# Performance work log

Measured on AMD Instinct MI355X. Metric: run time of the kernel, lower is better.

Reference implementation:

```python
import jax, jax.numpy as jnp
import numpy as np

N_EMBD = 1024
N_HEAD = 16
HEAD_DIM = N_EMBD // N_HEAD
BLOCK_SIZE = 2048
ROPE_BASE = 10000.0


def _rope_tables(dim, max_len, base=ROPE_BASE):
    half = dim // 2
    freqs = 1.0 / base ** (jnp.arange(half, dtype=jnp.float32) / half)
    angles = jnp.arange(max_len, dtype=jnp.float32)[:, None] * freqs[None, :]  # (T, half)
    return jnp.cos(angles), jnp.sin(angles)


def _apply_rope(x, cos, sin):
    # x: (B, H, T, D); cos/sin: (T, D//2)
    T = x.shape[2]
    c = cos[:T][None, None]
    s = sin[:T][None, None]
    x1 = x[..., ::2]
    x2 = x[..., 1::2]
    out = jnp.stack([x1 * c - x2 * s, x1 * s + x2 * c], axis=-1)  # (B,H,T,D//2,2)
    return out.reshape(x.shape)


def setup_inputs() -> dict:
    key = jax.random.key(0)
    k1, k2, k3, k4, k5 = jax.random.split(key, 5)
    B, T, C = 2, 2048, N_EMBD
    x = jax.random.normal(k1, (B, T, C), dtype=jnp.float32)
    scale = 1.0 / np.sqrt(C)
    Wqkv = jax.random.normal(k2, (C, 3 * C), dtype=jnp.float32) * scale
    bqkv = jax.random.normal(k3, (3 * C,), dtype=jnp.float32) * 0.01
    Wproj = jax.random.normal(k4, (C, C), dtype=jnp.float32) * scale
    bproj = jax.random.normal(k5, (C,), dtype=jnp.float32) * 0.01
    cos, sin = _rope_tables(HEAD_DIM, BLOCK_SIZE)
    return {"x": x, "Wqkv": Wqkv, "bqkv": bqkv, "Wproj": Wproj, "bproj": bproj,
            "cos": cos, "sin": sin}


def reference(x, Wqkv, bqkv, Wproj, bproj, cos, sin):
    B, T, C = x.shape
    H, D = N_HEAD, HEAD_DIM
    qkv = x @ Wqkv + bqkv  # (B,T,3C)
    q, k, v = jnp.split(qkv, 3, axis=-1)
    # (B,T,C) -> (B,H,T,D)
    q = q.reshape(B, T, H, D).transpose(0, 2, 1, 3)
    k = k.reshape(B, T, H, D).transpose(0, 2, 1, 3)
    v = v.reshape(B, T, H, D).transpose(0, 2, 1, 3)
    q = _apply_rope(q, cos, sin)
    k = _apply_rope(k, cos, sin)
    att = jnp.einsum('bhtd,bhsd->bhts', q, k) * (D ** -0.5)
    causal = jnp.tril(jnp.ones((T, T), dtype=bool))
    att = jnp.where(causal[None, None], att, -jnp.inf)
    att = jax.nn.softmax(att, axis=-1)
    y = jnp.einsum('bhts,bhsd->bhtd', att, v)  # (B,H,T,D)
    y = y.transpose(0, 2, 1, 3).reshape(B, T, C)
    return y @ Wproj + bproj
```

## Files before the change

### kernel.cpp

```cpp
#include <hip/hip_runtime.h>
#include <stdint.h>

typedef short s16x8 __attribute__((ext_vector_type(8)));
typedef float f32x4 __attribute__((ext_vector_type(4)));
typedef unsigned short u16;
typedef unsigned int u32;

__device__ __forceinline__ float bf2f(u16 u) {
  union { u32 i; float f; } v; v.i = ((u32)u) << 16; return v.f;
}
__device__ __forceinline__ u16 f2bf(float f) {
  union { float f; u32 i; } v; v.f = f;
  u32 i = v.i;
  return (u16)((i + 0x7fffu + ((i >> 16) & 1u)) >> 16);
}
__device__ __forceinline__ u16 f2bf_fast(float f) {
  union { float f; u32 i; } v; v.f = f;
  return (u16)((v.i + 0x8000u) >> 16);
}

__device__ __forceinline__ s16x8 load8(const void* p, size_t idx, int isf32) {
  s16x8 r;
  if (isf32) {
    const float* f = (const float*)p + idx;
    f32x4 a = *(const f32x4*)f;
    f32x4 b = *(const f32x4*)(f + 4);
#pragma unroll
    for (int j = 0; j < 4; j++) {
      r[j] = (short)f2bf(a[j]);
      r[4 + j] = (short)f2bf(b[j]);
    }
  } else {
    r = *(const s16x8*)((const u16*)p + idx);
  }
  return r;
}
__device__ __forceinline__ float loadf(const void* p, size_t idx, int isf32) {
  return isf32 ? ((const float*)p)[idx] : bf2f(((const u16*)p)[idx]);
}

__device__ __forceinline__ void cp16(const u16* g, u16* l) {
  __builtin_amdgcn_global_load_lds(
      (const __attribute__((address_space(1))) u32*)g,
      (__attribute__((address_space(3))) u32*)l, 16, 0, 0);
}

__global__ void detect_dtype(const u16* __restrict__ x, int* __restrict__ flags) {
  int cnt = 0;
  for (int i = threadIdx.x; i < 4096; i += 64) {
    int e = (x[i] >> 7) & 0xFF;
    if (e >= 0xF0) cnt++;
  }
  unsigned long long any = __ballot(cnt > 0);
  if (threadIdx.x == 0) {
    flags[0] = (any != 0ull) ? 1 : 0;
    flags[1] = 0;
  }
}

__global__ __launch_bounds__(256) void convert_x(const void* __restrict__ x,
                                                 const int* __restrict__ fp,
                                                 u16* __restrict__ xb) {
  int tid = blockIdx.x * 256 + threadIdx.x;
  int r = tid & 127, kq = (tid >> 7) & 3, kB = (tid >> 9) & 31, mB = tid >> 14;
  size_t src = (size_t)(mB * 128 + r) * 1024 + kB * 32 + kq * 8;
  *(s16x8*)(xb + (size_t)tid * 8) = load8(x, src, *fp);
}

__global__ __launch_bounds__(256) void transposeW2(
    const void* __restrict__ Wqkv, const void* __restrict__ Wproj,
    const int* __restrict__ fp, u16* __restrict__ WqkvT,
    u16* __restrict__ WprojT) {
  __shared__ u32 tile32[32 * 66];
  const int f = *fp;
  const int tid = threadIdx.x;
  const int bx = blockIdx.x;
  const void* W;
  u16* WT;
  int N, nb, qkvSide;
  if (bx < 48) { W = Wqkv; WT = WqkvT; N = 3072; nb = bx * 64; qkvSide = 1; }
  else         { W = Wproj; WT = WprojT; N = 1024; nb = (bx - 48) * 64; qkvSide = 0; }
  const int kb = blockIdx.y * 64;
  {
    int a = tid >> 3, c8 = tid & 7;
    s16x8 r0 = load8(W, (size_t)(kb + 2 * a) * N + nb + c8 * 8, f);
    s16x8 r1 = load8(W, (size_t)(kb + 2 * a + 1) * N + nb + c8 * 8, f);
#pragma unroll
    for (int j = 0; j < 8; j++)
      tile32[a * 66 + c8 * 8 + j] = (u32)(u16)r0[j] | ((u32)(u16)r1[j] << 16);
  }
  __syncthreads();
#pragma unroll
  for (int i = 0; i < 2; i++) {
    int idx = tid + i * 256;
    int n = idx & 63, c8 = idx >> 6;
    s16x8 v;
#pragma unroll
    for (int w = 0; w < 4; w++) {
      u32 pk = tile32[(c8 * 4 + w) * 66 + n];
      v[2 * w] = (short)(u16)(pk & 0xFFFF);
      v[2 * w + 1] = (short)(u16)(pk >> 16);
    }
    int R = nb + n, k = kb + c8 * 8;
    int kB = k >> 5, kq = (k >> 3) & 3;
    size_t off;
    if (qkvSide) {
      int nB = R >> 7, r = R & 127;
      off = ((size_t)(nB * 32 + kB) * 4 + kq) * 1024 + r * 8;
    } else {
      int nB = R >> 6, r = R & 63;
      off = (size_t)(nB * 32 + kB) * 2048 + kq * 512 + r * 8;
    }
    *(s16x8*)(WT + off) = v;
  }
}

__global__ __launch_bounds__(256) void transposeV(const u16* __restrict__ qkv,
                                                  u16* __restrict__ vT) {
  __shared__ u32 tile32[64 * 33];
  const int tid = threadIdx.x;
  const int tb = blockIdx.x * 64, bh = blockIdx.y;
  const int b = bh >> 4, h = bh & 15;
  {
    int a = tid >> 3, c8 = tid & 7;
    const u16* base = qkv + (size_t)(b * 2048 + tb + 2 * a) * 3072 + 2048 + h * 64;
    s16x8 r0 = *(const s16x8*)(base + c8 * 8);
    s16x8 r1 = *(const s16x8*)(base + 3072 + c8 * 8);
#pragma unroll
    for (int j = 0; j < 8; j++)
      tile32[(c8 * 8 + j) * 33 + a] = (u32)(u16)r0[j] | ((u32)(u16)r1[j] << 16);
  }
  __syncthreads();
#pragma unroll
  for (int i = 0; i < 2; i++) {
    int idx = tid + i * 256;
    int d = idx >> 3, c8 = idx & 7;
    s16x8 v;
#pragma unroll
    for (int w = 0; w < 4; w++) {
      u32 pk = tile32[d * 33 + c8 * 4 + w];
      v[2 * w] = (short)(u16)(pk & 0xFFFF);
      v[2 * w + 1] = (short)(u16)(pk >> 16);
    }
    *(s16x8*)(vT + ((size_t)bh * 64 + d) * 2048 + tb + c8 * 8) = v;
  }
}

template <int NT, int KK, int ATILED>
__global__ __launch_bounds__(256) void gemm_bt(
    const u16* __restrict__ A, int lda, const u16* __restrict__ Bt,
    const void* __restrict__ bias, const int* __restrict__ fI32,
    void* __restrict__ C, int ropeMode, int outF,
    const void* __restrict__ cost, const void* __restrict__ sint, int N) {
  constexpr int NTW = NT / 32;
  constexpr int KT = KK / 32;
  constexpr int TB = NT * 32;
  __shared__ __attribute__((aligned(16))) u16 As[128 * 32];
  __shared__ __attribute__((aligned(16))) u16 Bs[NT * 32];
  const int inf32 = *fI32;
  const int tid = threadIdx.x;
  const int wave = tid >> 6, lane = tid & 63, quad = lane >> 4, l16 = lane & 15;
  const int m0 = blockIdx.y * 128, n0 = blockIdx.x * NT;
  const int wm = (wave & 1) * 64, wn = (wave >> 1) * (NT / 2);
  f32x4 acc[4][NTW];
#pragma unroll
  for (int i = 0; i < 4; i++)
#pragma unroll
    for (int j = 0; j < NTW; j++) acc[i][j] = (f32x4){0.f, 0.f, 0.f, 0.f};

  const u16* aT = nullptr;
  const u16* aP = nullptr;
  if constexpr (ATILED) {
    aT = A + (size_t)blockIdx.y * KT * 4096 + wave * 1024 + lane * 8;
  } else {
    const int lr = lane >> 2, lk = (lane & 3) * 8;
    aP = A + (size_t)(m0 + wave * 32 + lr) * lda + lk;
  }
  const u16* bT = Bt + (size_t)blockIdx.x * KT * TB + wave * (NT / 64) * 512 +
                  lane * 8;

  for (int kB = 0; kB < KT; ++kB) {
    __syncthreads();
    if constexpr (ATILED) {
      cp16(aT + (size_t)kB * 4096, As + wave * 1024);
      cp16(aT + (size_t)kB * 4096 + 512, As + wave * 1024 + 512);
    } else {
      const int kb = kB * 32;
      cp16(aP + kb, As + wave * 32 * 32);
      cp16(aP + kb + (size_t)16 * lda, As + wave * 32 * 32 + 16 * 32);
    }
#pragma unroll
    for (int i = 0; i < NT / 64; i++)
      cp16(bT + (size_t)kB * TB + i * 512,
           Bs + (wave * (NT / 64) + i) * 512);
    __syncthreads();
    s16x8 af[4], bfr[NTW];
#pragma unroll
    for (int tt = 0; tt < 4; tt++) {
      if constexpr (ATILED)
        af[tt] = *(const s16x8*)(As + quad * 1024 + (wm + tt * 16 + l16) * 8);
      else
        af[tt] = *(const s16x8*)(As + (wm + tt * 16 + l16) * 32 + quad * 8);
    }
#pragma unroll
    for (int tt = 0; tt < NTW; tt++)
      bfr[tt] = *(const s16x8*)(Bs + quad * (NT * 8) + (wn + tt * 16 + l16) * 8);
#pragma unroll
    for (int mt = 0; mt < 4; mt++)
#pragma unroll
      for (int nt = 0; nt < NTW; nt++)
        acc[mt][nt] = __builtin_amdgcn_mfma_f32_16x16x32_bf16(
            af[mt], bfr[nt], acc[mt][nt], 0, 0, 0);
  }

#pragma unroll
  for (int nt = 0; nt < NTW; nt++) {
    int col = n0 + wn + nt * 16 + l16;
    float bv = loadf(bias, col, inf32);
    if (ropeMode && col < 2048) {
      int j = (col & 63) >> 1, odd = col & 1;
#pragma unroll
      for (int mt = 0; mt < 4; mt++)
#pragma unroll
        for (int r = 0; r < 4; r++) {
          int row = m0 + wm + mt * 16 + quad * 4 + r, t = row & 2047;
          float cv = loadf(cost, (size_t)t * 32 + j, inf32);
          float sv = loadf(sint, (size_t)t * 32 + j, inf32);
          float val = acc[mt][nt][r] + bv;
          float pr = __shfl_xor(val, 1);
          float res = odd ? (pr * sv + val * cv) : (val * cv - pr * sv);
          ((u16*)C)[(size_t)row * N + col] = f2bf(res);
        }
    } else if (outF && inf32) {
#pragma unroll
      for (int mt = 0; mt < 4; mt++)
#pragma unroll
        for (int r = 0; r < 4; r++) {
          int row = m0 + wm + mt * 16 + quad * 4 + r;
          ((float*)C)[(size_t)row * N + col] = acc[mt][nt][r] + bv;
        }
    } else {
#pragma unroll
      for (int mt = 0; mt < 4; mt++)
#pragma unroll
        for (int r = 0; r < 4; r++) {
          int row = m0 + wm + mt * 16 + quad * 4 + r;
          ((u16*)C)[(size_t)row * N + col] = f2bf(acc[mt][nt][r] + bv);
        }
    }
  }
}

__global__ __launch_bounds__(512) void attn_kernel(u16* qkv,
                                                   const u16* __restrict__ vT) {
  __shared__ __attribute__((aligned(16))) u16 Ks[64 * 72];
  __shared__ __attribute__((aligned(16))) u16 Vt[64 * 72];
  __shared__ __attribute__((aligned(16))) u16 Pl[8][16 * 72];
  const int tid = threadIdx.x;
  const int wave = tid >> 6, lane = tid & 63, quad = lane >> 4, l16 = lane & 15;
  const int cu = blockIdx.x & 255, round = blockIdx.x >> 8;
  const int p = cu >> 5, bh = cu & 31;
  const int qt = round ? p : 15 - p;
  const int h = bh & 15;
  const size_t rb = (size_t)(bh >> 4) * 2048;
  const int qb = qt * 128;
  const float SCALE = 0.18033688011112042f;

  s16x8 qa0, qa1;
  {
    const u16* qp = qkv + (rb + qb + wave * 16 + l16) * 3072 + h * 64;
    qa0 = *(const s16x8*)(qp + quad * 8);
    qa1 = *(const s16x8*)(qp + 32 + quad * 8);
  }

  f32x4 o[4];
  float l_r[4] = {0.f, 0.f, 0.f, 0.f};
#pragma unroll
  for (int i = 0; i < 4; i++) o[i] = (f32x4){0.f, 0.f, 0.f, 0.f};

  const int nchunks = 2 * qt + 2;
  const int srow = tid >> 3, sc8 = tid & 7;
  s16x8 kr, vr;
  {
    kr = *(const s16x8*)(qkv + (rb + srow) * 3072 + 1024 + h * 64 + sc8 * 8);
    vr = *(const s16x8*)(vT + ((size_t)bh * 64 + srow) * 2048 + sc8 * 8);
  }

  for (int c = 0; c < nchunks; c++) {
    const int sb = c * 64;
    __syncthreads();
    *(s16x8*)(Ks + srow * 72 + sc8 * 8) = kr;
    *(s16x8*)(Vt + srow * 72 + sc8 * 8) = vr;
    __syncthreads();
    if (c + 1 < nchunks) {
      const int nb = sb + 64;
      kr = *(const s16x8*)(qkv + (rb + nb + srow) * 3072 + 1024 + h * 64 +
                           sc8 * 8);
      vr = *(const s16x8*)(vT + ((size_t)bh * 64 + srow) * 2048 + nb + sc8 * 8);
    }

    if (sb > qb + wave * 16 + 15) continue;

    f32x4 S[4];
#pragma unroll
    for (int kf = 0; kf < 4; kf++) {
      s16x8 k0 = *(const s16x8*)(Ks + (kf * 16 + l16) * 72 + quad * 8);
      s16x8 k1 = *(const s16x8*)(Ks + (kf * 16 + l16) * 72 + 32 + quad * 8);
      f32x4 a = (f32x4){0.f, 0.f, 0.f, 0.f};
      a = __builtin_amdgcn_mfma_f32_16x16x32_bf16(qa0, k0, a, 0, 0, 0);
      a = __builtin_amdgcn_mfma_f32_16x16x32_bf16(qa1, k1, a, 0, 0, 0);
      S[kf] = a;
    }

    u16* P = Pl[wave];
    const int mq = qb + wave * 16;
    const bool needMask = (sb + 63) > mq;
#pragma unroll
    for (int r = 0; r < 4; r++) {
      const int qi = mq + quad * 4 + r;
#pragma unroll
      for (int kf = 0; kf < 4; kf++) {
        float pv = __builtin_amdgcn_exp2f(S[kf][r] * SCALE);
        if (needMask) pv = ((sb + kf * 16 + l16) <= qi) ? pv : 0.f;
        l_r[r] += pv;
        P[(quad * 4 + r) * 72 + kf * 16 + l16] = f2bf_fast(pv);
      }
    }
    asm volatile("s_waitcnt lgkmcnt(0)" ::: "memory");
    s16x8 pa0 = *(const s16x8*)(P + l16 * 72 + quad * 8);
    s16x8 pa1 = *(const s16x8*)(P + l16 * 72 + 32 + quad * 8);

#pragma unroll
    for (int dt = 0; dt < 4; dt++) {
      s16x8 vb0 = *(const s16x8*)(Vt + (dt * 16 + l16) * 72 + quad * 8);
      s16x8 vb1 = *(const s16x8*)(Vt + (dt * 16 + l16) * 72 + 32 + quad * 8);
      o[dt] = __builtin_amdgcn_mfma_f32_16x16x32_bf16(pa0, vb0, o[dt], 0, 0, 0);
      o[dt] = __builtin_amdgcn_mfma_f32_16x16x32_bf16(pa1, vb1, o[dt], 0, 0, 0);
    }
  }

  float inv[4];
#pragma unroll
  for (int r = 0; r < 4; r++) {
    float rs = l_r[r];
#pragma unroll
    for (int off = 8; off; off >>= 1) rs += __shfl_xor(rs, off);
    inv[r] = 1.0f / fmaxf(rs, 1e-30f);
  }
#pragma unroll
  for (int dt = 0; dt < 4; dt++)
#pragma unroll
    for (int r = 0; r < 4; r++)
      qkv[(rb + qb + wave * 16 + quad * 4 + r) * 3072 + 2048 + h * 64 +
          dt * 16 + l16] = f2bf(o[dt][r] * inv[r]);
}

extern "C" void kernel_launch(void* const* d_in, const int* in_sizes, int n_in,
                              void* d_out, int out_size, void* d_ws,
                              size_t ws_size, hipStream_t stream) {
  const void* x = d_in[0];
  const void* Wqkv = d_in[1];
  const void* bqkv = d_in[2];
  const void* Wproj = d_in[3];
  const void* bproj = d_in[4];
  const void* cost = d_in[5];
  const void* sint = d_in[6];

  int* flags = (int*)d_ws;
  u16* WqkvT = (u16*)d_ws + 128;
  u16* WprojT = WqkvT + (size_t)3072 * 1024;
  u16* qkv = WprojT + (size_t)1024 * 1024;
  u16* yb = qkv + 2048;
  u16* xb = (u16*)d_out;
  u16* vT = (u16*)d_out + (size_t)4096 * 1024;

  detect_dtype<<<1, 64, 0, stream>>>((const u16*)x, flags);
  convert_x<<<2048, 256, 0, stream>>>(x, flags, xb);
  transposeW2<<<dim3(64, 16), 256, 0, stream>>>(Wqkv, Wproj, flags, WqkvT,
                                                WprojT);
  gemm_bt<128, 1024, 1><<<dim3(24, 32), 256, 0, stream>>>(
      xb, 1024, WqkvT, bqkv, flags, qkv, 1, 0, cost, sint, 3072);
  transposeV<<<dim3(32, 32), 256, 0, stream>>>(qkv, vT);
  attn_kernel<<<512, 512, 0, stream>>>(qkv, vT);
  gemm_bt<64, 1024, 0><<<dim3(16, 32), 256, 0, stream>>>(
      yb, 3072, WprojT, bproj, flags, d_out, 0, 1, nullptr, nullptr, 1024);
}
```

Measured before the change: 218.3 us.

## Double-buffer GEMM LDS tiles and remap blocks per XCD for locality

Converts the GEMM K-loop to a double-buffered LDS pipeline: the async copy for the next K-slice is issued before computing the current one, with explicit vmcnt waits and barriers in place of two __syncthreads per iteration. It also remaps the linear block ID so that blocks assigned round-robin to each of the 8 XCDs cover a contiguous region of the output grid, aiming for better L2 reuse of A and B tiles. LDS use doubles, which may reduce occupancy. The hand-written vmcnt counts and the grid remap both assume particular shapes: the grid must divide into 2x4 regions, and the counts must match the number of cp16 instructions issued per stage.

```diff
diff --git a/kernel.cpp b/kernel.cpp
--- a/kernel.cpp
+++ b/kernel.cpp
@@ -155,12 +155,21 @@
   constexpr int NTW = NT / 32;
   constexpr int KT = KK / 32;
   constexpr int TB = NT * 32;
-  __shared__ __attribute__((aligned(16))) u16 As[128 * 32];
-  __shared__ __attribute__((aligned(16))) u16 Bs[NT * 32];
+  __shared__ __attribute__((aligned(16))) u16 As[2][128 * 32];
+  __shared__ __attribute__((aligned(16))) u16 Bs[2][NT * 32];
   const int inf32 = *fI32;
   const int tid = threadIdx.x;
   const int wave = tid >> 6, lane = tid & 63, quad = lane >> 4, l16 = lane & 15;
-  const int m0 = blockIdx.y * 128, n0 = blockIdx.x * NT;
+
+  const int GX = gridDim.x;
+  const int lin = blockIdx.y * GX + blockIdx.x;
+  const int xcd = lin & 7, idx = lin >> 3;
+  const int RX = GX >> 1, RY = gridDim.y >> 2;
+  const int sx = idx % RX, sy = idx / RX;
+  const int bx = (xcd & 1) * RX + sx;
+  const int by = (xcd >> 1) * RY + sy;
+
+  const int m0 = by * 128, n0 = bx * NT;
   const int wm = (wave & 1) * 64, wn = (wave >> 1) * (NT / 2);
   f32x4 acc[4][NTW];
 #pragma unroll
@@ -171,46 +180,67 @@
   const u16* aT = nullptr;
   const u16* aP = nullptr;
   if constexpr (ATILED) {
-    aT = A + (size_t)blockIdx.y * KT * 4096 + wave * 1024 + lane * 8;
+    aT = A + (size_t)by * KT * 4096 + wave * 1024 + lane * 8;
   } else {
     const int lr = lane >> 2, lk = (lane & 3) * 8;
     aP = A + (size_t)(m0 + wave * 32 + lr) * lda + lk;
   }
-  const u16* bT = Bt + (size_t)blockIdx.x * KT * TB + wave * (NT / 64) * 512 +
+  const u16* bT = Bt + (size_t)bx * KT * TB + wave * (NT / 64) * 512 +
                   lane * 8;
 
-  for (int kB = 0; kB < KT; ++kB) {
-    __syncthreads();
+  auto STAGE = [&](int kB, u16* ad, u16* bd) {
     if constexpr (ATILED) {
-      cp16(aT + (size_t)kB * 4096, As + wave * 1024);
-      cp16(aT + (size_t)kB * 4096 + 512, As + wave * 1024 + 512);
+      cp16(aT + (size_t)kB * 4096, ad + wave * 1024);
+      cp16(aT + (size_t)kB * 4096 + 512, ad + wave * 1024 + 512);
     } else {
       const int kb = kB * 32;
-      cp16(aP + kb, As + wave * 32 * 32);
-      cp16(aP + kb + (size_t)16 * lda, As + wave * 32 * 32 + 16 * 32);
+      cp16(aP + kb, ad + wave * 1024);
+      cp16(aP + kb + (size_t)16 * lda, ad + wave * 1024 + 512);
     }
 #pragma unroll
     for (int i = 0; i < NT / 64; i++)
-      cp16(bT + (size_t)kB * TB + i * 512,
-           Bs + (wave * (NT / 64) + i) * 512);
-    __syncthreads();
+      cp16(bT + (size_t)kB * TB + i * 512, bd + (wave * (NT / 64) + i) * 512);
+  };
+
+  u16 *aCur = &As[0][0], *aNxt = &As[1][0];
+  u16 *bCur = &Bs[0][0], *bNxt = &Bs[1][0];
+  STAGE(0, aCur, bCur);
+
+  for (int t = 0; t < KT; ++t) {
+    if (t + 1 < KT) {
+      STAGE(t + 1, aNxt, bNxt);
+      if constexpr (NT == 128) asm volatile("s_waitcnt vmcnt(4)" ::: "memory");
+      else                     asm volatile("s_waitcnt vmcnt(3)" ::: "memory");
+    } else {
+      asm volatile("s_waitcnt vmcnt(0)" ::: "memory");
+    }
+    __builtin_amdgcn_s_barrier();
+    __builtin_amdgcn_sched_barrier(0);
+
     s16x8 af[4], bfr[NTW];
 #pragma unroll
     for (int tt = 0; tt < 4; tt++) {
       if constexpr (ATILED)
-        af[tt] = *(const s16x8*)(As + quad * 1024 + (wm + tt * 16 + l16) * 8);
+        af[tt] = *(const s16x8*)(aCur + quad * 1024 + (wm + tt * 16 + l16) * 8);
       else
-        af[tt] = *(const s16x8*)(As + (wm + tt * 16 + l16) * 32 + quad * 8);
+        af[tt] = *(const s16x8*)(aCur + (wm + tt * 16 + l16) * 32 + quad * 8);
     }
 #pragma unroll
     for (int tt = 0; tt < NTW; tt++)
-      bfr[tt] = *(const s16x8*)(Bs + quad * (NT * 8) + (wn + tt * 16 + l16) * 8);
+      bfr[tt] = *(const s16x8*)(bCur + quad * (NT * 8) + (wn + tt * 16 + l16) * 8);
 #pragma unroll
     for (int mt = 0; mt < 4; mt++)
 #pragma unroll
       for (int nt = 0; nt < NTW; nt++)
         acc[mt][nt] = __builtin_amdgcn_mfma_f32_16x16x32_bf16(
             af[mt], bfr[nt], acc[mt][nt], 0, 0, 0);
+
+    asm volatile("s_waitcnt lgkmcnt(0)" ::: "memory");
+    __builtin_amdgcn_sched_barrier(0);
+    __builtin_amdgcn_s_barrier();
+    u16* tp;
+    tp = aCur; aCur = aNxt; aNxt = tp;
+    tp = bCur; bCur = bNxt; bNxt = tp;
   }
 
 #pragma unroll
```

Result: no change. 214.2 us (-1.8%).

## Deepen QKV GEMM K-step to 64 and swizzle blocks across XCDs

Applied to the files above, without the earlier changes.

The QKV projection GEMM now stages a 64-wide K slice per iteration, running two MFMA sub-steps per pair of barriers, which halves the number of synchronizations and global-load rounds. It also remaps the linear block ID so that blocks landing on the same XCD cover a contiguous sub-rectangle of the output, aiming for better L2 reuse of A and B tiles. The output projection keeps BK=32 and no swizzle. The cost is doubled LDS use for the QKV GEMM, which may lower occupancy, and the swizzle assumes grid dimensions divisible by 2 and 4.

```diff
diff --git a/kernel.cpp b/kernel.cpp
--- a/kernel.cpp
+++ b/kernel.cpp
@@ -146,21 +146,40 @@
   }
 }
 
-template <int NT, int KK, int ATILED>
+template <int NT, int KK, int ATILED, int BK, int SWZ>
 __global__ __launch_bounds__(256) void gemm_bt(
     const u16* __restrict__ A, int lda, const u16* __restrict__ Bt,
     const void* __restrict__ bias, const int* __restrict__ fI32,
     void* __restrict__ C, int ropeMode, int outF,
     const void* __restrict__ cost, const void* __restrict__ sint, int N) {
   constexpr int NTW = NT / 32;
-  constexpr int KT = KK / 32;
-  constexpr int TB = NT * 32;
-  __shared__ __attribute__((aligned(16))) u16 As[128 * 32];
-  __shared__ __attribute__((aligned(16))) u16 Bs[NT * 32];
+  constexpr int KSUB = BK / 32;
+  constexpr int KT = KK / BK;
+  constexpr int AE = 128 * BK;
+  constexpr int BE = NT * BK;
+  constexpr int APW = AE / 2048;
+  constexpr int BPW = BE / 2048;
+  __shared__ __attribute__((aligned(16))) u16 As[AE];
+  __shared__ __attribute__((aligned(16))) u16 Bs[BE];
   const int inf32 = *fI32;
   const int tid = threadIdx.x;
   const int wave = tid >> 6, lane = tid & 63, quad = lane >> 4, l16 = lane & 15;
-  const int m0 = blockIdx.y * 128, n0 = blockIdx.x * NT;
+
+  int bx, by;
+  if constexpr (SWZ) {
+    const int GX = gridDim.x;
+    const int lin = blockIdx.y * GX + blockIdx.x;
+    const int xcd = lin & 7, idx = lin >> 3;
+    const int RX = GX >> 1, RY = gridDim.y >> 2;
+    const int sx = idx % RX, sy = idx / RX;
+    bx = (xcd & 1) * RX + sx;
+    by = (xcd >> 1) * RY + sy;
+  } else {
+    bx = blockIdx.x;
+    by = blockIdx.y;
+  }
+
+  const int m0 = by * 128, n0 = bx * NT;
   const int wm = (wave & 1) * 64, wn = (wave >> 1) * (NT / 2);
   f32x4 acc[4][NTW];
 #pragma unroll
@@ -171,46 +190,52 @@
   const u16* aT = nullptr;
   const u16* aP = nullptr;
   if constexpr (ATILED) {
-    aT = A + (size_t)blockIdx.y * KT * 4096 + wave * 1024 + lane * 8;
+    aT = A + (size_t)by * KK * 128 + lane * 8;
   } else {
     const int lr = lane >> 2, lk = (lane & 3) * 8;
     aP = A + (size_t)(m0 + wave * 32 + lr) * lda + lk;
   }
-  const u16* bT = Bt + (size_t)blockIdx.x * KT * TB + wave * (NT / 64) * 512 +
-                  lane * 8;
-
-  for (int kB = 0; kB < KT; ++kB) {
+  const u16* bT = Bt + (size_t)bx * KK * NT + lane * 8;
+
+  for (int s = 0; s < KT; ++s) {
     __syncthreads();
     if constexpr (ATILED) {
-      cp16(aT + (size_t)kB * 4096, As + wave * 1024);
-      cp16(aT + (size_t)kB * 4096 + 512, As + wave * 1024 + 512);
+#pragma unroll
+      for (int j = 0; j < APW; j++)
+        cp16(aT + (size_t)s * AE + (wave * APW + j) * 512,
+             As + (wave * APW + j) * 512);
     } else {
-      const int kb = kB * 32;
-      cp16(aP + kb, As + wave * 32 * 32);
-      cp16(aP + kb + (size_t)16 * lda, As + wave * 32 * 32 + 16 * 32);
-    }
-#pragma unroll
-    for (int i = 0; i < NT / 64; i++)
-      cp16(bT + (size_t)kB * TB + i * 512,
-           Bs + (wave * (NT / 64) + i) * 512);
+      const int kb = s * 32;
+      cp16(aP + kb, As + wave * 1024);
+      cp16(aP + kb + (size_t)16 * lda, As + wave * 1024 + 512);
+    }
+#pragma unroll
+    for (int j = 0; j < BPW; j++)
+      cp16(bT + (size_t)s * BE + (wave * BPW + j) * 512,
+           Bs + (wave * BPW + j) * 512);
     __syncthreads();
-    s16x8 af[4], bfr[NTW];
-#pragma unroll
-    for (int tt = 0; tt < 4; tt++) {
-      if constexpr (ATILED)
-        af[tt] = *(const s16x8*)(As + quad * 1024 + (wm + tt * 16 + l16) * 8);
-      else
-        af[tt] = *(const s16x8*)(As + (wm + tt * 16 + l16) * 32 + quad * 8);
-    }
-#pragma unroll
-    for (int tt = 0; tt < NTW; tt++)
-      bfr[tt] = *(const s16x8*)(Bs + quad * (NT * 8) + (wn + tt * 16 + l16) * 8);
-#pragma unroll
-    for (int mt = 0; mt < 4; mt++)
-#pragma unroll
-      for (int nt = 0; nt < NTW; nt++)
-        acc[mt][nt] = __builtin_amdgcn_mfma_f32_16x16x32_bf16(
-            af[mt], bfr[nt], acc[mt][nt], 0, 0, 0);
+#pragma unroll
+    for (int ks = 0; ks < KSUB; ks++) {
+      s16x8 af[4], bfr[NTW];
+#pragma unroll
+      for (int tt = 0; tt < 4; tt++) {
+        if constexpr (ATILED)
+          af[tt] = *(const s16x8*)(As + ks * 4096 + quad * 1024 +
+                                   (wm + tt * 16 + l16) * 8);
+        else
+          af[tt] = *(const s16x8*)(As + (wm + tt * 16 + l16) * 32 + quad * 8);
+      }
+#pragma unroll
+      for (int tt = 0; tt < NTW; tt++)
+        bfr[tt] = *(const s16x8*)(Bs + ks * (NT * 32) + quad * (NT * 8) +
+                                  (wn + tt * 16 + l16) * 8);
+#pragma unroll
+      for (int mt = 0; mt < 4; mt++)
+#pragma unroll
+        for (int nt = 0; nt < NTW; nt++)
+          acc[mt][nt] = __builtin_amdgcn_mfma_f32_16x16x32_bf16(
+              af[mt], bfr[nt], acc[mt][nt], 0, 0, 0);
+    }
   }
 
 #pragma unroll
@@ -378,10 +403,10 @@
   convert_x<<<2048, 256, 0, stream>>>(x, flags, xb);
   transposeW2<<<dim3(64, 16), 256, 0, stream>>>(Wqkv, Wproj, flags, WqkvT,
                                                 WprojT);
-  gemm_bt<128, 1024, 1><<<dim3(24, 32), 256, 0, stream>>>(
+  gemm_bt<128, 1024, 1, 64, 1><<<dim3(24, 32), 256, 0, stream>>>(
       xb, 1024, WqkvT, bqkv, flags, qkv, 1, 0, cost, sint, 3072);
   transposeV<<<dim3(32, 32), 256, 0, stream>>>(qkv, vT);
   attn_kernel<<<512, 512, 0, stream>>>(qkv, vT);
-  gemm_bt<64, 1024, 0><<<dim3(16, 32), 256, 0, stream>>>(
+  gemm_bt<64, 1024, 0, 32, 0><<<dim3(16, 32), 256, 0, stream>>>(
       yb, 3072, WprojT, bproj, flags, d_out, 0, 1, nullptr, nullptr, 1024);
 }
```

Result: no change. 217.4 us (-0.4%).
